# Kernel tuning notes

Hardware: AMD Instinct MI355X
Metric: run time of the kernel (lower is better)

## Reference

```python
import jax, jax.numpy as jnp
import numpy as np

E, D, H, W = 512, 64, 64, 64
B, L = 8, 2048
STEPS = 5
OUT_SIGMA_SCALE = 2.0


def setup_inputs() -> dict:
    key = jax.random.key(0)
    ks = jax.random.split(key, 8)
    tokens = jax.random.normal(ks[0], (B, L, E), dtype=jnp.float32)
    # positions on the HxW lattice: col 0 in [0,H), col 1 in [0,W)
    pos = jax.random.uniform(ks[1], (B, L, 2), dtype=jnp.float32)
    positions = pos * jnp.array([H, W], dtype=jnp.float32)
    # learned params (fan-in scaled init, as nn.Linear/Conv2d would give)
    W_to_field = jax.random.normal(ks[2], (D, E), dtype=jnp.float32) / np.sqrt(E)
    W_from_field = jax.random.normal(ks[3], (E, D), dtype=jnp.float32) / np.sqrt(D)
    conv1_w = jax.random.normal(ks[4], (2 * D, D, 3, 3), dtype=jnp.float32) / np.sqrt(D * 9)
    conv1_b = jnp.zeros((2 * D,), dtype=jnp.float32)
    conv2_w = jax.random.normal(ks[5], (D, 2 * D, 1, 1), dtype=jnp.float32) / np.sqrt(2 * D)
    conv2_b = jnp.zeros((D,), dtype=jnp.float32)
    log_sigma = jnp.array(np.log(4.0), dtype=jnp.float32)
    return {
        "tokens": tokens, "positions": positions,
        "W_to_field": W_to_field, "W_from_field": W_from_field,
        "conv1_w": conv1_w, "conv1_b": conv1_b,
        "conv2_w": conv2_w, "conv2_b": conv2_b,
        "log_sigma": log_sigma,
    }


def _conv2d(x, w, b, pad):
    y = jax.lax.conv_general_dilated(
        x, w, window_strides=(1, 1), padding=[(pad, pad), (pad, pad)],
        dimension_numbers=("NCHW", "OIHW", "NCHW"))
    return y + b[None, :, None, None]


def _norm_gauss(dy2, dx2, sigma):
    # (B,L,H,1)+(B,L,1,W) -> (B,L,H,W), normalized over the lattice
    g = jnp.exp(-(dy2 + dx2) / (2.0 * sigma * sigma))
    return g / (jnp.sum(g, axis=(-2, -1), keepdims=True) + 1e-6)


def reference(tokens, positions, W_to_field, W_from_field,
              conv1_w, conv1_b, conv2_w, conv2_b, log_sigma):
    sigma_in = jax.nn.softplus(log_sigma) + 1e-6
    sigma_out = sigma_in * OUT_SIGMA_SCALE

    proj = jnp.einsum("ble,de->bld", tokens, W_to_field)  # (B,L,D)

    grid_y = jnp.arange(H, dtype=jnp.float32)  # (H,)
    grid_x = jnp.arange(W, dtype=jnp.float32)  # (W,)
    dy2 = (grid_y[None, None, :, None] - positions[..., 0][..., None, None]) ** 2  # (B,L,H,1)
    dx2 = (grid_x[None, None, None, :] - positions[..., 1][..., None, None]) ** 2  # (B,L,1,W)

    weights_in = _norm_gauss(dy2, dx2, sigma_in)   # (B,L,H,W)
    field = jnp.einsum("blc,blhw->bchw", proj, weights_in)  # (B,D,H,W)

    for _ in range(STEPS):
        h = jax.nn.relu(_conv2d(field, conv1_w, conv1_b, pad=1))
        field = field + _conv2d(h, conv2_w, conv2_b, pad=0)

    weights_out = _norm_gauss(dy2, dx2, sigma_out)  # (B,L,H,W)
    sampled = jnp.einsum("bchw,blhw->blc", field, weights_out)  # (B,L,D)

    tokens_out = jnp.einsum("bld,ed->ble", sampled, W_from_field)  # (B,L,E)
    return tokens_out
```

## Files before the change

kernel.cpp:

```cpp
#include <hip/hip_runtime.h>
#include <cmath>
#include <cstddef>

#define BB 8
#define LL 2048
#define EE 512
#define HW 4096

typedef __attribute__((ext_vector_type(8))) short short8;
typedef __attribute__((ext_vector_type(4))) short short4v;
typedef __attribute__((ext_vector_type(4))) float f32x4;

__device__ __forceinline__ int swz(int row, int k, int ldk) {
    int g = (k >> 3) ^ (row & ((ldk >> 3) - 1));
    return row * ldk + (g << 3) + (k & 7);
}
__device__ __forceinline__ unsigned short f2bf(float f) {
    unsigned u = __builtin_bit_cast(unsigned, f);
    return (unsigned short)((u + 0x7FFFu + ((u >> 16) & 1u)) >> 16);
}
__device__ __forceinline__ float bf2f(short s) {
    return __builtin_bit_cast(float, (unsigned)((unsigned short)s) << 16);
}
__device__ __forceinline__ short4v cvt4(float4 v) {
    short4v r;
    r[0] = (short)f2bf(v.x); r[1] = (short)f2bf(v.y);
    r[2] = (short)f2bf(v.z); r[3] = (short)f2bf(v.w);
    return r;
}
#define MFMA16(acc, a, b) acc = __builtin_amdgcn_mfma_f32_16x16x32_bf16(a, b, acc, 0, 0, 0)

__global__ __launch_bounds__(256) void k_gauss(const float* __restrict__ pos,
        const float* __restrict__ lsig,
        short* __restrict__ gyiT, short* __restrict__ gxiT,
        short* __restrict__ gyoT, short* __restrict__ gxo,
        const float* __restrict__ w1, const float* __restrict__ w2,
        short* __restrict__ w1b, short* __restrict__ w2b) {
    __shared__ float red[4][4][64];
    __shared__ float tile[64 * 65];
    int t = threadIdx.x;
    int bx = blockIdx.x;
    {
        int i = bx * 256 + t;
        if (i < 73728) {
            int c = i & 63, o = (i >> 6) & 127, tap = i >> 13;
            w1b[i] = (short)f2bf(w1[(size_t)o * 576 + c * 9 + tap]);
        }
        if (i < 8192) w2b[i] = (short)f2bf(w2[i]);
    }
    if (bx >= 256) return;
    int ll = t & 63, q = t >> 6;
    int b = bx >> 5, lt = bx & 31;
    int bl = b * LL + lt * 64 + ll;
    float py = pos[(size_t)bl * 2 + 0];
    float px = pos[(size_t)bl * 2 + 1];
    float ls = lsig[0];
    float si = log1pf(expf(ls)) + 1e-6f;
    float so = si * 2.0f;
    float ai = 0.5f / (si * si), ao = 0.5f / (so * so);
    float vyi[16], vxi[16], vyo[16], vxo[16];
    float pyi = 0.f, pxi = 0.f, pyo = 0.f, pxo = 0.f;
    #pragma unroll
    for (int j = 0; j < 16; j++) {
        float g = (float)(q * 16 + j);
        float dy = g - py, dx = g - px;
        float dy2 = dy * dy, dx2 = dx * dx;
        vyi[j] = expf(-dy2 * ai); pyi += vyi[j];
        vxi[j] = expf(-dx2 * ai); pxi += vxi[j];
        vyo[j] = expf(-dy2 * ao); pyo += vyo[j];
        vxo[j] = expf(-dx2 * ao); pxo += vxo[j];
    }
    red[0][q][ll] = pyi; red[1][q][ll] = pxi;
    red[2][q][ll] = pyo; red[3][q][ll] = pxo;
    __syncthreads();
    float syi = red[0][0][ll] + red[0][1][ll] + red[0][2][ll] + red[0][3][ll];
    float sxi = red[1][0][ll] + red[1][1][ll] + red[1][2][ll] + red[1][3][ll];
    float syo = red[2][0][ll] + red[2][1][ll] + red[2][2][ll] + red[2][3][ll];
    float sxo = red[3][0][ll] + red[3][1][ll] + red[3][2][ll] + red[3][3][ll];
    float inv_i = 1.0f / (syi * sxi + 1e-6f);
    float inv_o = 1.0f / (syo * sxo + 1e-6f);
    size_t base = (size_t)b * 64 * LL + lt * 64 + ll;
    #pragma unroll
    for (int j = 0; j < 16; j++) {
        size_t off = base + (size_t)(q * 16 + j) * LL;
        gyiT[off] = (short)f2bf(vyi[j] * inv_i);
        gxiT[off] = (short)f2bf(vxi[j]);
        gyoT[off] = (short)f2bf(vyo[j] * inv_o);
        tile[(q * 16 + j) * 65 + ll] = vxo[j];
    }
    __syncthreads();
    #pragma unroll
    for (int j = 0; j < 16; j++) {
        int i = t + 256 * j;
        int lo = i >> 6, wo = i & 63;
        gxo[((size_t)b * LL + lt * 64 + lo) * 64 + wo] = (short)f2bf(tile[wo * 65 + lo]);
    }
}

__global__ __launch_bounds__(256) void k_proj(const float* __restrict__ tokens,
        const float* __restrict__ wtf, short* __restrict__ projT) {
    __shared__ __align__(16) short At[4096], Bt[4096];
    int t = threadIdx.x, lane = t & 63, wid = t >> 6;
    int blk = blockIdx.x;
    int b = blk >> 5;
    int l0b = (blk & 31) * 64;
    size_t tokbase = ((size_t)b * LL + l0b) * EE;
    f32x4 z = {0.f, 0.f, 0.f, 0.f};
    f32x4 acc[4] = {z, z, z, z};
    float4 pa[4], pb[4];
    #pragma unroll
    for (int j = 0; j < 4; j++) {
        int idx = t + 256 * j;
        int row = idx >> 4, kq = (idx & 15) << 2;
        pa[j] = *(const float4*)&wtf[(size_t)row * EE + kq];
        pb[j] = *(const float4*)&tokens[tokbase + (size_t)row * EE + kq];
    }
    for (int c = 0; c < 8; c++) {
        __syncthreads();
        #pragma unroll
        for (int j = 0; j < 4; j++) {
            int idx = t + 256 * j;
            int row = idx >> 4, kq = (idx & 15) << 2;
            *(short4v*)&At[swz(row, kq, 64)] = cvt4(pa[j]);
            *(short4v*)&Bt[swz(row, kq, 64)] = cvt4(pb[j]);
        }
        __syncthreads();
        if (c < 7) {
            int e0 = (c + 1) * 64;
            #pragma unroll
            for (int j = 0; j < 4; j++) {
                int idx = t + 256 * j;
                int row = idx >> 4, kq = (idx & 15) << 2;
                pa[j] = *(const float4*)&wtf[(size_t)row * EE + e0 + kq];
                pb[j] = *(const float4*)&tokens[tokbase + (size_t)row * EE + e0 + kq];
            }
        }
        int mrow = wid * 16 + (lane & 15);
        #pragma unroll
        for (int ks = 0; ks < 2; ks++) {
            int k0 = ks * 32 + (lane >> 4) * 8;
            short8 a = *(short8*)&At[swz(mrow, k0, 64)];
            #pragma unroll
            for (int n = 0; n < 4; n++) {
                short8 bb = *(short8*)&Bt[swz(n * 16 + (lane & 15), k0, 64)];
                MFMA16(acc[n], a, bb);
            }
        }
    }
    #pragma unroll
    for (int n = 0; n < 4; n++)
        #pragma unroll
        for (int r = 0; r < 4; r++) {
            int d = wid * 16 + ((lane >> 4) << 2) + r;
            int l = l0b + n * 16 + (lane & 15);
            projT[((size_t)b * 64 + d) * LL + l] = (short)f2bf(acc[n][r]);
        }
}

__global__ __launch_bounds__(256, 3) void k_scatter(const short* __restrict__ projT,
        const short* __restrict__ gyiT, const short* __restrict__ gxiT,
        float* __restrict__ fz) {
    __shared__ __align__(16) char smem[49152];
    short* At = (short*)smem;
    short* B0 = At + 8192;
    short* B1 = B0 + 8192;
    float* Cf = (float*)smem;
    const size_t FP = (size_t)BB * 64 * HW;
    int t = threadIdx.x, lane = t & 63, wid = t >> 6;
    int hp = blockIdx.x, b = blockIdx.y, kz = blockIdx.z;
    int h0 = hp * 2;
    const short* pj  = projT + (size_t)b * 64 * LL + kz * 1024;
    const short* gx  = gxiT + (size_t)b * 64 * LL + kz * 1024;
    const short* gy0 = gyiT + ((size_t)b * 64 + h0) * LL + kz * 1024;
    const short* gy1 = gy0 + LL;
    f32x4 z = {0.f, 0.f, 0.f, 0.f};
    f32x4 acc0[4] = {z, z, z, z}, acc1[4] = {z, z, z, z};
    int row_ = t >> 4, g_ = t & 15;
    short8 pA[4], pX[4], pY0v, pY1v;
    pY0v = *(const short8*)&gy0[g_ * 8];
    pY1v = *(const short8*)&gy1[g_ * 8];
    #pragma unroll
    for (int j = 0; j < 4; j++) {
        int row = row_ + 16 * j;
        pA[j] = *(const short8*)&pj[(size_t)row * LL + g_ * 8];
        pX[j] = *(const short8*)&gx[(size_t)row * LL + g_ * 8];
    }
    for (int c = 0; c < 8; c++) {
        __syncthreads();
        #pragma unroll
        for (int j = 0; j < 4; j++) {
            int row = row_ + 16 * j;
            short8 b0v, b1v;
            #pragma unroll
            for (int e = 0; e < 8; e++) {
                float gxv = bf2f(pX[j][e]);
                b0v[e] = (short)f2bf(gxv * bf2f(pY0v[e]));
                b1v[e] = (short)f2bf(gxv * bf2f(pY1v[e]));
            }
            *(short8*)&At[swz(row, g_ * 8, 128)] = pA[j];
            *(short8*)&B0[swz(row, g_ * 8, 128)] = b0v;
            *(short8*)&B1[swz(row, g_ * 8, 128)] = b1v;
        }
        __syncthreads();
        if (c < 7) {
            int off = (c + 1) * 128;
            pY0v = *(const short8*)&gy0[off + g_ * 8];
            pY1v = *(const short8*)&gy1[off + g_ * 8];
            #pragma unroll
            for (int j = 0; j < 4; j++) {
                int row = row_ + 16 * j;
                pA[j] = *(const short8*)&pj[(size_t)row * LL + off + g_ * 8];
                pX[j] = *(const short8*)&gx[(size_t)row * LL + off + g_ * 8];
            }
        }
        int mrow = wid * 16 + (lane & 15);
        #pragma unroll
        for (int ks = 0; ks < 4; ks++) {
            int k0 = ks * 32 + (lane >> 4) * 8;
            short8 a = *(short8*)&At[swz(mrow, k0, 128)];
            #pragma unroll
            for (int n = 0; n < 4; n++) {
                short8 b0f = *(short8*)&B0[swz(n * 16 + (lane & 15), k0, 128)];
                short8 b1f = *(short8*)&B1[swz(n * 16 + (lane & 15), k0, 128)];
                MFMA16(acc0[n], a, b0f);
                MFMA16(acc1[n], a, b1f);
            }
        }
    }
    float* dst = fz + (size_t)kz * FP;
    #pragma unroll
    for (int p = 0; p < 2; p++) {
        __syncthreads();
        #pragma unroll
        for (int n = 0; n < 4; n++)
            #pragma unroll
            for (int r = 0; r < 4; r++) {
                int w = n * 16 + (lane & 15);
                int cc = wid * 16 + ((lane >> 4) << 2) + r;
                Cf[w * 68 + cc] = (p == 0) ? acc0[n][r] : acc1[n][r];
            }
        __syncthreads();
        #pragma unroll
        for (int j = 0; j < 4; j++) {
            int i = t + 256 * j;
            int wo = i >> 4, cq = (i & 15) << 2;
            *(float4*)&dst[(((size_t)b * 64 + h0 + p) * 64 + wo) * 64 + cq] =
                *(float4*)&Cf[wo * 68 + cq];
        }
    }
}

__global__ __launch_bounds__(256, 3) void k_conv(const float* __restrict__ fin,
        int nparts, float* __restrict__ fout,
        const short* __restrict__ w1b, const float* __restrict__ b1,
        const short* __restrict__ w2b, const float* __restrict__ b2,
        short* __restrict__ fnchw, int final_step) {
    __shared__ __align__(16) char smem[45568];
    short* halo = (short*)smem;
    short* w1t  = (short*)(smem + 12800);
    short* ht   = (short*)(smem + 29184);
    float* Cf   = (float*)smem;
    const size_t FP = (size_t)BB * 64 * HW;
    int t = threadIdx.x, lane = t & 63, wid = t >> 6;
    int tile = blockIdx.x, b = blockIdx.y;
    int y0 = (tile >> 3) << 3, x0 = (tile & 7) << 3;
    const float* fb = fin + (size_t)b * 64 * HW;

    short8 w2f[4][4];
    #pragma unroll
    for (int n = 0; n < 4; n++)
        #pragma unroll
        for (int ks = 0; ks < 4; ks++)
            w2f[n][ks] = *(const short8*)&w2b[(size_t)(n * 16 + (lane & 15)) * 128
                                              + ks * 32 + (lane >> 4) * 8];
    short8 pf[4];
    #pragma unroll
    for (int j = 0; j < 4; j++) {
        int i = t + 256 * j; int o = i >> 3, g = i & 7;
        pf[j] = *(const short8*)&w1b[(size_t)o * 64 + g * 8];
    }
    for (int i = t; i < 1600; i += 256) {
        int pix = i >> 4, cq = (i & 15) << 2;
        int pr = pix / 10, pc = pix - pr * 10;
        int gy = y0 + pr - 1, gx = x0 + pc - 1;
        float4 v = {0.f, 0.f, 0.f, 0.f};
        if ((unsigned)gy < 64u && (unsigned)gx < 64u) {
            size_t a = ((size_t)gy * 64 + gx) * 64 + cq;
            v = *(const float4*)&fb[a];
            for (int p = 1; p < nparts; p++) {
                float4 u = *(const float4*)&fb[(size_t)p * FP + a];
                v.x += u.x; v.y += u.y; v.z += u.z; v.w += u.w;
            }
        }
        *(short4v*)&halo[swz(pix, cq, 64)] = cvt4(v);
    }
    f32x4 accH[8];
    #pragma unroll
    for (int n = 0; n < 8; n++) {
        float bv = b1[n * 16 + (lane & 15)];
        f32x4 v = {bv, bv, bv, bv};
        accH[n] = v;
    }
    int mpix = wid * 16 + (lane & 15);
    int ppy = mpix >> 3, ppx = mpix & 7;

    #pragma unroll
    for (int tap = 0; tap < 9; tap++) {
        #pragma unroll
        for (int j = 0; j < 4; j++) {
            int i = t + 256 * j; int o = i >> 3, g = i & 7;
            *(short8*)&w1t[swz(o, g * 8, 64)] = pf[j];
        }
        if (tap < 8) {
            #pragma unroll
            for (int j = 0; j < 4; j++) {
                int i = t + 256 * j; int o = i >> 3, g = i & 7;
                pf[j] = *(const short8*)&w1b[((size_t)(tap + 1) * 128 + o) * 64 + g * 8];
            }
        }
        __syncthreads();
        int ky = tap / 3, kx = tap - ky * 3;
        int hpix = (ppy + ky) * 10 + (ppx + kx);
        #pragma unroll
        for (int ks = 0; ks < 2; ks++) {
            int k0 = ks * 32 + (lane >> 4) * 8;
            short8 a = *(short8*)&halo[swz(hpix, k0, 64)];
            #pragma unroll
            for (int n = 0; n < 8; n++) {
                short8 bb = *(short8*)&w1t[swz(n * 16 + (lane & 15), k0, 64)];
                MFMA16(accH[n], a, bb);
            }
        }
        __syncthreads();
    }
    #pragma unroll
    for (int n = 0; n < 8; n++)
        #pragma unroll
        for (int r = 0; r < 4; r++) {
            int m = wid * 16 + ((lane >> 4) << 2) + r;
            int o = n * 16 + (lane & 15);
            ht[swz(m, o, 128)] = (short)f2bf(fmaxf(accH[n][r], 0.f));
        }
    __syncthreads();
    f32x4 acc2[4];
    #pragma unroll
    for (int n = 0; n < 4; n++) {
        float bv = b2[n * 16 + (lane & 15)];
        f32x4 v = {bv, bv, bv, bv};
        acc2[n] = v;
    }
    #pragma unroll
    for (int ks = 0; ks < 4; ks++) {
        int k0 = ks * 32 + (lane >> 4) * 8;
        short8 a = *(short8*)&ht[swz(mpix, k0, 128)];
        #pragma unroll
        for (int n = 0; n < 4; n++) MFMA16(acc2[n], a, w2f[n][ks]);
    }
    float* fo = fout + (size_t)b * 64 * HW;
    #pragma unroll
    for (int n = 0; n < 4; n++)
        #pragma unroll
        for (int r = 0; r < 4; r++) {
            int m = wid * 16 + ((lane >> 4) << 2) + r;
            int py = m >> 3, px = m & 7;
            int d = n * 16 + (lane & 15);
            size_t a = (((size_t)(y0 + py)) * 64 + x0 + px) * 64 + d;
            float fv = fb[a];
            for (int p = 1; p < nparts; p++) fv += fb[(size_t)p * FP + a];
            float val = acc2[n][r] + fv;
            if (!final_step) fo[a] = val;
            else Cf[d * 68 + m] = val;
        }
    if (final_step) {
        __syncthreads();
        #pragma unroll
        for (int j = 0; j < 4; j++) {
            int i = t + 256 * j;
            int d = i >> 4, pq = (i & 15) << 2;
            int py = pq >> 3, px = pq & 7;
            float4 v = *(float4*)&Cf[d * 68 + pq];
            *(short4v*)&fnchw[(((size_t)b * 64 + d) * 64 + y0 + py) * 64 + x0 + px] =
                cvt4(v);
        }
    }
}

__global__ __launch_bounds__(256, 4) void k_gather(const short* __restrict__ fnchw,
        const short* __restrict__ gyoT, const short* __restrict__ gxo,
        float* __restrict__ sampz) {
    __shared__ __align__(16) short At[8192], Bt[8192];
    int t = threadIdx.x, lane = t & 63, wid = t >> 6;
    int lt = blockIdx.x, b = blockIdx.y, zz = blockIdx.z;
    int l0 = lt * 64;
    f32x4 z4 = {0.f, 0.f, 0.f, 0.f};
    f32x4 acc[4] = {z4, z4, z4, z4};
    int row_ = t >> 4, g_ = t & 15;
    int hl_ = g_ >> 3, w8_ = (g_ & 7) * 8;
    short8 pX[4], pB[4];
    float pY[4];
    #pragma unroll
    for (int j = 0; j < 4; j++) {
        int row = row_ + 16 * j;
        int h = zz * 16 + hl_;
        pX[j] = *(const short8*)&gxo[((size_t)b * LL + l0 + row) * 64 + w8_];
        pY[j] = bf2f(gyoT[((size_t)b * 64 + h) * LL + l0 + row]);
        pB[j] = *(const short8*)&fnchw[(((size_t)b * 64 + row) * 64 + h) * 64 + w8_];
    }
    for (int c = 0; c < 8; c++) {
        __syncthreads();
        #pragma unroll
        for (int j = 0; j < 4; j++) {
            int row = row_ + 16 * j;
            short8 a;
            #pragma unroll
            for (int e = 0; e < 8; e++)
                a[e] = (short)f2bf(bf2f(pX[j][e]) * pY[j]);
            *(short8*)&At[swz(row, g_ * 8, 128)] = a;
            *(short8*)&Bt[swz(row, g_ * 8, 128)] = pB[j];
        }
        __syncthreads();
        if (c < 7) {
            int h = zz * 16 + (c + 1) * 2 + hl_;
            #pragma unroll
            for (int j = 0; j < 4; j++) {
                int row = row_ + 16 * j;
                pY[j] = bf2f(gyoT[((size_t)b * 64 + h) * LL + l0 + row]);
                pB[j] = *(const short8*)&fnchw[(((size_t)b * 64 + row) * 64 + h) * 64 + w8_];
            }
        }
        int mrow = wid * 16 + (lane & 15);
        #pragma unroll
        for (int ks = 0; ks < 4; ks++) {
            int k0 = ks * 32 + (lane >> 4) * 8;
            short8 a = *(short8*)&At[swz(mrow, k0, 128)];
            #pragma unroll
            for (int n = 0; n < 4; n++) {
                short8 bb = *(short8*)&Bt[swz(n * 16 + (lane & 15), k0, 128)];
                MFMA16(acc[n], a, bb);
            }
        }
    }
    #pragma unroll
    for (int n = 0; n < 4; n++)
        #pragma unroll
        for (int r = 0; r < 4; r++) {
            int lr = wid * 16 + ((lane >> 4) << 2) + r;
            int cc = n * 16 + (lane & 15);
            sampz[(((size_t)zz * BB + b) * LL + l0 + lr) * 64 + cc] = acc[n][r];
        }
}

__global__ __launch_bounds__(256) void k_out(const float* __restrict__ samp,
        const float* __restrict__ wff, float* __restrict__ out) {
    __shared__ __align__(16) short At[4096], Bt[4096];
    const size_t SP = 1048576;
    int t = threadIdx.x, lane = t & 63, wid = t >> 6;
    int mt = blockIdx.x, e0 = blockIdx.y * 64;
    #pragma unroll
    for (int j = 0; j < 4; j++) {
        int idx = t + 256 * j;
        int row = idx >> 4, kq = (idx & 15) << 2;
        size_t off = ((size_t)mt * 64 + row) * 64 + kq;
        float4 v0 = *(const float4*)&samp[off];
        float4 v1 = *(const float4*)&samp[off + SP];
        float4 v2 = *(const float4*)&samp[off + 2 * SP];
        float4 v3 = *(const float4*)&samp[off + 3 * SP];
        float4 vs = {v0.x + v1.x + v2.x + v3.x, v0.y + v1.y + v2.y + v3.y,
                     v0.z + v1.z + v2.z + v3.z, v0.w + v1.w + v2.w + v3.w};
        *(short4v*)&At[swz(row, kq, 64)] = cvt4(vs);
        float4 wv = *(const float4*)&wff[(size_t)(e0 + row) * 64 + kq];
        *(short4v*)&Bt[swz(row, kq, 64)] = cvt4(wv);
    }
    __syncthreads();
    f32x4 z = {0.f, 0.f, 0.f, 0.f};
    f32x4 acc[4] = {z, z, z, z};
    int mrow = wid * 16 + (lane & 15);
    #pragma unroll
    for (int ks = 0; ks < 2; ks++) {
        int k0 = ks * 32 + (lane >> 4) * 8;
        short8 a = *(short8*)&At[swz(mrow, k0, 64)];
        #pragma unroll
        for (int n = 0; n < 4; n++) {
            short8 bb = *(short8*)&Bt[swz(n * 16 + (lane & 15), k0, 64)];
            MFMA16(acc[n], a, bb);
        }
    }
    #pragma unroll
    for (int n = 0; n < 4; n++)
        #pragma unroll
        for (int r = 0; r < 4; r++) {
            int lr = wid * 16 + ((lane >> 4) << 2) + r;
            int ec = e0 + n * 16 + (lane & 15);
            out[((size_t)mt * 64 + lr) * EE + ec] = acc[n][r];
        }
}

extern "C" void kernel_launch(void* const* d_in, const int* in_sizes, int n_in,
                              void* d_out, int out_size, void* d_ws, size_t ws_size,
                              hipStream_t stream) {
    const float* tokens = (const float*)d_in[0];
    const float* pos    = (const float*)d_in[1];
    const float* wtf    = (const float*)d_in[2];
    const float* wff    = (const float*)d_in[3];
    const float* w1     = (const float*)d_in[4];
    const float* b1     = (const float*)d_in[5];
    const float* w2     = (const float*)d_in[6];
    const float* b2     = (const float*)d_in[7];
    const float* lsig   = (const float*)d_in[8];
    float* out = (float*)d_out;

    const size_t M1 = 1048576;
    float* ws    = (float*)d_ws;
    short* sbase = (short*)d_ws;
    short* gyiT  = sbase;
    short* gxiT  = sbase + 1 * M1;
    short* gyoT  = sbase + 2 * M1;
    short* gxo   = sbase + 3 * M1;
    short* projT = sbase + 4 * M1;
    float* fz    = ws + 3 * M1;
    float* fA    = ws + 7 * M1;
    float* fB    = ws + 9 * M1;
    short* fnchw = (short*)(ws + 11 * M1);
    float* samp  = ws + 12 * M1;
    short* w1b   = (short*)(ws + 16 * M1);
    short* w2b   = w1b + 73728;

    hipLaunchKernelGGL(k_gauss, dim3(288), dim3(256), 0, stream,
                       pos, lsig, gyiT, gxiT, gyoT, gxo, w1, w2, w1b, w2b);
    hipLaunchKernelGGL(k_proj, dim3(256), dim3(256), 0, stream, tokens, wtf, projT);
    hipLaunchKernelGGL(k_scatter, dim3(32, 8, 2), dim3(256), 0, stream,
                       projT, gyiT, gxiT, fz);
    hipLaunchKernelGGL(k_conv, dim3(64, 8), dim3(256), 0, stream,
                       fz, 2, fB, w1b, b1, w2b, b2, fnchw, 0);
    hipLaunchKernelGGL(k_conv, dim3(64, 8), dim3(256), 0, stream,
                       fB, 1, fA, w1b, b1, w2b, b2, fnchw, 0);
    hipLaunchKernelGGL(k_conv, dim3(64, 8), dim3(256), 0, stream,
                       fA, 1, fB, w1b, b1, w2b, b2, fnchw, 0);
    hipLaunchKernelGGL(k_conv, dim3(64, 8), dim3(256), 0, stream,
                       fB, 1, fA, w1b, b1, w2b, b2, fnchw, 0);
    hipLaunchKernelGGL(k_conv, dim3(64, 8), dim3(256), 0, stream,
                       fA, 1, fB, w1b, b1, w2b, b2, fnchw, 1);
    hipLaunchKernelGGL(k_gather, dim3(32, 8, 4), dim3(256), 0, stream,
                       fnchw, gyoT, gxo, samp);
    hipLaunchKernelGGL(k_out, dim3(256, 8), dim3(256), 0, stream,
                       samp, wff, out);
}
```

Baseline: 244.1 us.

## Fuse projection into gauss kernel and double split-K for scatter and gather

Merges the token projection GEMM into the gaussian-weights kernel as extra blocks, so both run in one launch and can overlap. Doubles the split-K factor of the scatter kernel (2 to 4 partial fields) and of the gather kernel (4 to 8 partial samples) to launch more blocks on a large GPU. In exchange, the conv and output kernels must read and sum more partial buffers, and the fused kernel's larger shared memory footprint may lower occupancy of the gauss blocks.

```diff
diff --git a/kernel.cpp b/kernel.cpp
--- a/kernel.cpp
+++ b/kernel.cpp
@@ -30,16 +30,79 @@
 }
 #define MFMA16(acc, a, b) acc = __builtin_amdgcn_mfma_f32_16x16x32_bf16(a, b, acc, 0, 0, 0)
 
-__global__ __launch_bounds__(256) void k_gauss(const float* __restrict__ pos,
+__global__ __launch_bounds__(256) void k_gauss_proj(const float* __restrict__ pos,
         const float* __restrict__ lsig,
         short* __restrict__ gyiT, short* __restrict__ gxiT,
         short* __restrict__ gyoT, short* __restrict__ gxo,
         const float* __restrict__ w1, const float* __restrict__ w2,
-        short* __restrict__ w1b, short* __restrict__ w2b) {
+        short* __restrict__ w1b, short* __restrict__ w2b,
+        const float* __restrict__ tokens, const float* __restrict__ wtf,
+        short* __restrict__ projT) {
     __shared__ float red[4][4][64];
     __shared__ float tile[64 * 65];
+    __shared__ __align__(16) short At[4096], Bt[4096];
     int t = threadIdx.x;
     int bx = blockIdx.x;
+
+    if (bx >= 288) {
+        int blk = bx - 288;
+        int lane = t & 63, wid = t >> 6;
+        int b = blk >> 5;
+        int l0b = (blk & 31) * 64;
+        size_t tokbase = ((size_t)b * LL + l0b) * EE;
+        f32x4 z = {0.f, 0.f, 0.f, 0.f};
+        f32x4 acc[4] = {z, z, z, z};
+        float4 pa[4], pb[4];
+        #pragma unroll
+        for (int j = 0; j < 4; j++) {
+            int idx = t + 256 * j;
+            int row = idx >> 4, kq = (idx & 15) << 2;
+            pa[j] = *(const float4*)&wtf[(size_t)row * EE + kq];
+            pb[j] = *(const float4*)&tokens[tokbase + (size_t)row * EE + kq];
+        }
+        for (int c = 0; c < 8; c++) {
+            __syncthreads();
+            #pragma unroll
+            for (int j = 0; j < 4; j++) {
+                int idx = t + 256 * j;
+                int row = idx >> 4, kq = (idx & 15) << 2;
+                *(short4v*)&At[swz(row, kq, 64)] = cvt4(pa[j]);
+                *(short4v*)&Bt[swz(row, kq, 64)] = cvt4(pb[j]);
+            }
+            __syncthreads();
+            if (c < 7) {
+                int e0 = (c + 1) * 64;
+                #pragma unroll
+                for (int j = 0; j < 4; j++) {
+                    int idx = t + 256 * j;
+                    int row = idx >> 4, kq = (idx & 15) << 2;
+                    pa[j] = *(const float4*)&wtf[(size_t)row * EE + e0 + kq];
+                    pb[j] = *(const float4*)&tokens[tokbase + (size_t)row * EE + e0 + kq];
+                }
+            }
+            int mrow = wid * 16 + (lane & 15);
+            #pragma unroll
+            for (int ks = 0; ks < 2; ks++) {
+                int k0 = ks * 32 + (lane >> 4) * 8;
+                short8 a = *(short8*)&At[swz(mrow, k0, 64)];
+                #pragma unroll
+                for (int n = 0; n < 4; n++) {
+                    short8 bb = *(short8*)&Bt[swz(n * 16 + (lane & 15), k0, 64)];
+                    MFMA16(acc[n], a, bb);
+                }
+            }
+        }
+        #pragma unroll
+        for (int n = 0; n < 4; n++)
+            #pragma unroll
+            for (int r = 0; r < 4; r++) {
+                int d = wid * 16 + ((lane >> 4) << 2) + r;
+                int l = l0b + n * 16 + (lane & 15);
+                projT[((size_t)b * 64 + d) * LL + l] = (short)f2bf(acc[n][r]);
+            }
+        return;
+    }
+
     {
         int i = bx * 256 + t;
         if (i < 73728) {
@@ -97,66 +160,6 @@
     }
 }
 
-__global__ __launch_bounds__(256) void k_proj(const float* __restrict__ tokens,
-        const float* __restrict__ wtf, short* __restrict__ projT) {
-    __shared__ __align__(16) short At[4096], Bt[4096];
-    int t = threadIdx.x, lane = t & 63, wid = t >> 6;
-    int blk = blockIdx.x;
-    int b = blk >> 5;
-    int l0b = (blk & 31) * 64;
-    size_t tokbase = ((size_t)b * LL + l0b) * EE;
-    f32x4 z = {0.f, 0.f, 0.f, 0.f};
-    f32x4 acc[4] = {z, z, z, z};
-    float4 pa[4], pb[4];
-    #pragma unroll
-    for (int j = 0; j < 4; j++) {
-        int idx = t + 256 * j;
-        int row = idx >> 4, kq = (idx & 15) << 2;
-        pa[j] = *(const float4*)&wtf[(size_t)row * EE + kq];
-        pb[j] = *(const float4*)&tokens[tokbase + (size_t)row * EE + kq];
-    }
-    for (int c = 0; c < 8; c++) {
-        __syncthreads();
-        #pragma unroll
-        for (int j = 0; j < 4; j++) {
-            int idx = t + 256 * j;
-            int row = idx >> 4, kq = (idx & 15) << 2;
-            *(short4v*)&At[swz(row, kq, 64)] = cvt4(pa[j]);
-            *(short4v*)&Bt[swz(row, kq, 64)] = cvt4(pb[j]);
-        }
-        __syncthreads();
-        if (c < 7) {
-            int e0 = (c + 1) * 64;
-            #pragma unroll
-            for (int j = 0; j < 4; j++) {
-                int idx = t + 256 * j;
-                int row = idx >> 4, kq = (idx & 15) << 2;
-                pa[j] = *(const float4*)&wtf[(size_t)row * EE + e0 + kq];
-                pb[j] = *(const float4*)&tokens[tokbase + (size_t)row * EE + e0 + kq];
-            }
-        }
-        int mrow = wid * 16 + (lane & 15);
-        #pragma unroll
-        for (int ks = 0; ks < 2; ks++) {
-            int k0 = ks * 32 + (lane >> 4) * 8;
-            short8 a = *(short8*)&At[swz(mrow, k0, 64)];
-            #pragma unroll
-            for (int n = 0; n < 4; n++) {
-                short8 bb = *(short8*)&Bt[swz(n * 16 + (lane & 15), k0, 64)];
-                MFMA16(acc[n], a, bb);
-            }
-        }
-    }
-    #pragma unroll
-    for (int n = 0; n < 4; n++)
-        #pragma unroll
-        for (int r = 0; r < 4; r++) {
-            int d = wid * 16 + ((lane >> 4) << 2) + r;
-            int l = l0b + n * 16 + (lane & 15);
-            projT[((size_t)b * 64 + d) * LL + l] = (short)f2bf(acc[n][r]);
-        }
-}
-
 __global__ __launch_bounds__(256, 3) void k_scatter(const short* __restrict__ projT,
         const short* __restrict__ gyiT, const short* __restrict__ gxiT,
         float* __restrict__ fz) {
@@ -169,9 +172,9 @@
     int t = threadIdx.x, lane = t & 63, wid = t >> 6;
     int hp = blockIdx.x, b = blockIdx.y, kz = blockIdx.z;
     int h0 = hp * 2;
-    const short* pj  = projT + (size_t)b * 64 * LL + kz * 1024;
-    const short* gx  = gxiT + (size_t)b * 64 * LL + kz * 1024;
-    const short* gy0 = gyiT + ((size_t)b * 64 + h0) * LL + kz * 1024;
+    const short* pj  = projT + (size_t)b * 64 * LL + kz * 512;
+    const short* gx  = gxiT + (size_t)b * 64 * LL + kz * 512;
+    const short* gy0 = gyiT + ((size_t)b * 64 + h0) * LL + kz * 512;
     const short* gy1 = gy0 + LL;
     f32x4 z = {0.f, 0.f, 0.f, 0.f};
     f32x4 acc0[4] = {z, z, z, z}, acc1[4] = {z, z, z, z};
@@ -185,7 +188,7 @@
         pA[j] = *(const short8*)&pj[(size_t)row * LL + g_ * 8];
         pX[j] = *(const short8*)&gx[(size_t)row * LL + g_ * 8];
     }
-    for (int c = 0; c < 8; c++) {
+    for (int c = 0; c < 4; c++) {
         __syncthreads();
         #pragma unroll
         for (int j = 0; j < 4; j++) {
@@ -202,7 +205,7 @@
             *(short8*)&B1[swz(row, g_ * 8, 128)] = b1v;
         }
         __syncthreads();
-        if (c < 7) {
+        if (c < 3) {
             int off = (c + 1) * 128;
             pY0v = *(const short8*)&gy0[off + g_ * 8];
             pY1v = *(const short8*)&gy1[off + g_ * 8];
@@ -401,12 +404,12 @@
     #pragma unroll
     for (int j = 0; j < 4; j++) {
         int row = row_ + 16 * j;
-        int h = zz * 16 + hl_;
+        int h = zz * 8 + hl_;
         pX[j] = *(const short8*)&gxo[((size_t)b * LL + l0 + row) * 64 + w8_];
         pY[j] = bf2f(gyoT[((size_t)b * 64 + h) * LL + l0 + row]);
         pB[j] = *(const short8*)&fnchw[(((size_t)b * 64 + row) * 64 + h) * 64 + w8_];
     }
-    for (int c = 0; c < 8; c++) {
+    for (int c = 0; c < 4; c++) {
         __syncthreads();
         #pragma unroll
         for (int j = 0; j < 4; j++) {
@@ -419,8 +422,8 @@
             *(short8*)&Bt[swz(row, g_ * 8, 128)] = pB[j];
         }
         __syncthreads();
-        if (c < 7) {
-            int h = zz * 16 + (c + 1) * 2 + hl_;
+        if (c < 3) {
+            int h = zz * 8 + (c + 1) * 2 + hl_;
             #pragma unroll
             for (int j = 0; j < 4; j++) {
                 int row = row_ + 16 * j;
@@ -461,12 +464,12 @@
         int idx = t + 256 * j;
         int row = idx >> 4, kq = (idx & 15) << 2;
         size_t off = ((size_t)mt * 64 + row) * 64 + kq;
-        float4 v0 = *(const float4*)&samp[off];
-        float4 v1 = *(const float4*)&samp[off + SP];
-        float4 v2 = *(const float4*)&samp[off + 2 * SP];
-        float4 v3 = *(const float4*)&samp[off + 3 * SP];
-        float4 vs = {v0.x + v1.x + v2.x + v3.x, v0.y + v1.y + v2.y + v3.y,
-                     v0.z + v1.z + v2.z + v3.z, v0.w + v1.w + v2.w + v3.w};
+        float4 vs = {0.f, 0.f, 0.f, 0.f};
+        #pragma unroll
+        for (int zp = 0; zp < 8; zp++) {
+            float4 v = *(const float4*)&samp[off + (size_t)zp * SP];
+            vs.x += v.x; vs.y += v.y; vs.z += v.z; vs.w += v.w;
+        }
         *(short4v*)&At[swz(row, kq, 64)] = cvt4(vs);
         float4 wv = *(const float4*)&wff[(size_t)(e0 + row) * 64 + kq];
         *(short4v*)&Bt[swz(row, kq, 64)] = cvt4(wv);
@@ -518,20 +521,20 @@
     short* gxo   = sbase + 3 * M1;
     short* projT = sbase + 4 * M1;
     float* fz    = ws + 3 * M1;
-    float* fA    = ws + 7 * M1;
-    float* fB    = ws + 9 * M1;
-    short* fnchw = (short*)(ws + 11 * M1);
-    float* samp  = ws + 12 * M1;
-    short* w1b   = (short*)(ws + 16 * M1);
+    float* fA    = ws + 11 * M1;
+    float* fB    = ws + 13 * M1;
+    short* fnchw = (short*)(ws + 15 * M1);
+    float* samp  = ws + 16 * M1;
+    short* w1b   = (short*)(ws + 24 * M1);
     short* w2b   = w1b + 73728;
 
-    hipLaunchKernelGGL(k_gauss, dim3(288), dim3(256), 0, stream,
-                       pos, lsig, gyiT, gxiT, gyoT, gxo, w1, w2, w1b, w2b);
-    hipLaunchKernelGGL(k_proj, dim3(256), dim3(256), 0, stream, tokens, wtf, projT);
-    hipLaunchKernelGGL(k_scatter, dim3(32, 8, 2), dim3(256), 0, stream,
+    hipLaunchKernelGGL(k_gauss_proj, dim3(544), dim3(256), 0, stream,
+                       pos, lsig, gyiT, gxiT, gyoT, gxo, w1, w2, w1b, w2b,
+                       tokens, wtf, projT);
+    hipLaunchKernelGGL(k_scatter, dim3(32, 8, 4), dim3(256), 0, stream,
                        projT, gyiT, gxiT, fz);
     hipLaunchKernelGGL(k_conv, dim3(64, 8), dim3(256), 0, stream,
-                       fz, 2, fB, w1b, b1, w2b, b2, fnchw, 0);
+                       fz, 4, fB, w1b, b1, w2b, b2, fnchw, 0);
     hipLaunchKernelGGL(k_conv, dim3(64, 8), dim3(256), 0, stream,
                        fB, 1, fA, w1b, b1, w2b, b2, fnchw, 0);
     hipLaunchKernelGGL(k_conv, dim3(64, 8), dim3(256), 0, stream,
@@ -540,7 +543,7 @@
                        fB, 1, fA, w1b, b1, w2b, b2, fnchw, 0);
     hipLaunchKernelGGL(k_conv, dim3(64, 8), dim3(256), 0, stream,
                        fA, 1, fB, w1b, b1, w2b, b2, fnchw, 1);
-    hipLaunchKernelGGL(k_gather, dim3(32, 8, 4), dim3(256), 0, stream,
+    hipLaunchKernelGGL(k_gather, dim3(32, 8, 8), dim3(256), 0, stream,
                        fnchw, gyoT, gxo, samp);
     hipLaunchKernelGGL(k_out, dim3(256, 8), dim3(256), 0, stream,
                        samp, wff, out);
```

Result: slower. 268.0 us (+9.8%).

## Merge gauss and projection kernels; put batch index fastest in grid order

Applied to the files above, without the earlier changes.

The projection GEMM now runs inside the Gaussian-table kernel as extra blocks (index 288 and up), so the two independent stages share one launch and can overlap. Every other kernel now takes the batch index from blockIdx.x, which reorders block dispatch so consecutive blocks span different batches. The merged kernel's shared memory grows to hold both stages' buffers, which may lower occupancy, and the new dispatch order changes L2 and XCD locality in ways that are hard to predict.

```diff
diff --git a/kernel.cpp b/kernel.cpp
--- a/kernel.cpp
+++ b/kernel.cpp
@@ -30,16 +30,79 @@
 }
 #define MFMA16(acc, a, b) acc = __builtin_amdgcn_mfma_f32_16x16x32_bf16(a, b, acc, 0, 0, 0)
 
-__global__ __launch_bounds__(256) void k_gauss(const float* __restrict__ pos,
+__global__ __launch_bounds__(256) void k_gauss_proj(const float* __restrict__ pos,
         const float* __restrict__ lsig,
         short* __restrict__ gyiT, short* __restrict__ gxiT,
         short* __restrict__ gyoT, short* __restrict__ gxo,
         const float* __restrict__ w1, const float* __restrict__ w2,
-        short* __restrict__ w1b, short* __restrict__ w2b) {
+        short* __restrict__ w1b, short* __restrict__ w2b,
+        const float* __restrict__ tokens, const float* __restrict__ wtf,
+        short* __restrict__ projT) {
     __shared__ float red[4][4][64];
     __shared__ float tile[64 * 65];
+    __shared__ __align__(16) short At[4096], Bt[4096];
     int t = threadIdx.x;
     int bx = blockIdx.x;
+
+    if (bx >= 288) {
+        int blk = bx - 288;
+        int lane = t & 63, wid = t >> 6;
+        int b = blk >> 5;
+        int l0b = (blk & 31) * 64;
+        size_t tokbase = ((size_t)b * LL + l0b) * EE;
+        f32x4 z = {0.f, 0.f, 0.f, 0.f};
+        f32x4 acc[4] = {z, z, z, z};
+        float4 pa[4], pb[4];
+        #pragma unroll
+        for (int j = 0; j < 4; j++) {
+            int idx = t + 256 * j;
+            int row = idx >> 4, kq = (idx & 15) << 2;
+            pa[j] = *(const float4*)&wtf[(size_t)row * EE + kq];
+            pb[j] = *(const float4*)&tokens[tokbase + (size_t)row * EE + kq];
+        }
+        for (int c = 0; c < 8; c++) {
+            __syncthreads();
+            #pragma unroll
+            for (int j = 0; j < 4; j++) {
+                int idx = t + 256 * j;
+                int row = idx >> 4, kq = (idx & 15) << 2;
+                *(short4v*)&At[swz(row, kq, 64)] = cvt4(pa[j]);
+                *(short4v*)&Bt[swz(row, kq, 64)] = cvt4(pb[j]);
+            }
+            __syncthreads();
+            if (c < 7) {
+                int e0 = (c + 1) * 64;
+                #pragma unroll
+                for (int j = 0; j < 4; j++) {
+                    int idx = t + 256 * j;
+                    int row = idx >> 4, kq = (idx & 15) << 2;
+                    pa[j] = *(const float4*)&wtf[(size_t)row * EE + e0 + kq];
+                    pb[j] = *(const float4*)&tokens[tokbase + (size_t)row * EE + e0 + kq];
+                }
+            }
+            int mrow = wid * 16 + (lane & 15);
+            #pragma unroll
+            for (int ks = 0; ks < 2; ks++) {
+                int k0 = ks * 32 + (lane >> 4) * 8;
+                short8 a = *(short8*)&At[swz(mrow, k0, 64)];
+                #pragma unroll
+                for (int n = 0; n < 4; n++) {
+                    short8 bb = *(short8*)&Bt[swz(n * 16 + (lane & 15), k0, 64)];
+                    MFMA16(acc[n], a, bb);
+                }
+            }
+        }
+        #pragma unroll
+        for (int n = 0; n < 4; n++)
+            #pragma unroll
+            for (int r = 0; r < 4; r++) {
+                int d = wid * 16 + ((lane >> 4) << 2) + r;
+                int l = l0b + n * 16 + (lane & 15);
+                projT[((size_t)b * 64 + d) * LL + l] = (short)f2bf(acc[n][r]);
+            }
+        return;
+    }
+
     {
         int i = bx * 256 + t;
         if (i < 73728) {
@@ -97,66 +160,6 @@
     }
 }
 
-__global__ __launch_bounds__(256) void k_proj(const float* __restrict__ tokens,
-        const float* __restrict__ wtf, short* __restrict__ projT) {
-    __shared__ __align__(16) short At[4096], Bt[4096];
-    int t = threadIdx.x, lane = t & 63, wid = t >> 6;
-    int blk = blockIdx.x;
-    int b = blk >> 5;
-    int l0b = (blk & 31) * 64;
-    size_t tokbase = ((size_t)b * LL + l0b) * EE;
-    f32x4 z = {0.f, 0.f, 0.f, 0.f};
-    f32x4 acc[4] = {z, z, z, z};
-    float4 pa[4], pb[4];
-    #pragma unroll
-    for (int j = 0; j < 4; j++) {
-        int idx = t + 256 * j;
-        int row = idx >> 4, kq = (idx & 15) << 2;
-        pa[j] = *(const float4*)&wtf[(size_t)row * EE + kq];
-        pb[j] = *(const float4*)&tokens[tokbase + (size_t)row * EE + kq];
-    }
-    for (int c = 0; c < 8; c++) {
-        __syncthreads();
-        #pragma unroll
-        for (int j = 0; j < 4; j++) {
-            int idx = t + 256 * j;
-            int row = idx >> 4, kq = (idx & 15) << 2;
-            *(short4v*)&At[swz(row, kq, 64)] = cvt4(pa[j]);
-            *(short4v*)&Bt[swz(row, kq, 64)] = cvt4(pb[j]);
-        }
-        __syncthreads();
-        if (c < 7) {
-            int e0 = (c + 1) * 64;
-            #pragma unroll
-            for (int j = 0; j < 4; j++) {
-                int idx = t + 256 * j;
-                int row = idx >> 4, kq = (idx & 15) << 2;
-                pa[j] = *(const float4*)&wtf[(size_t)row * EE + e0 + kq];
-                pb[j] = *(const float4*)&tokens[tokbase + (size_t)row * EE + e0 + kq];
-            }
-        }
-        int mrow = wid * 16 + (lane & 15);
-        #pragma unroll
-        for (int ks = 0; ks < 2; ks++) {
-            int k0 = ks * 32 + (lane >> 4) * 8;
-            short8 a = *(short8*)&At[swz(mrow, k0, 64)];
-            #pragma unroll
-            for (int n = 0; n < 4; n++) {
-                short8 bb = *(short8*)&Bt[swz(n * 16 + (lane & 15), k0, 64)];
-                MFMA16(acc[n], a, bb);
-            }
-        }
-    }
-    #pragma unroll
-    for (int n = 0; n < 4; n++)
-        #pragma unroll
-        for (int r = 0; r < 4; r++) {
-            int d = wid * 16 + ((lane >> 4) << 2) + r;
-            int l = l0b + n * 16 + (lane & 15);
-            projT[((size_t)b * 64 + d) * LL + l] = (short)f2bf(acc[n][r]);
-        }
-}
-
 __global__ __launch_bounds__(256, 3) void k_scatter(const short* __restrict__ projT,
         const short* __restrict__ gyiT, const short* __restrict__ gxiT,
         float* __restrict__ fz) {
@@ -167,7 +170,7 @@
     float* Cf = (float*)smem;
     const size_t FP = (size_t)BB * 64 * HW;
     int t = threadIdx.x, lane = t & 63, wid = t >> 6;
-    int hp = blockIdx.x, b = blockIdx.y, kz = blockIdx.z;
+    int b = blockIdx.x, hp = blockIdx.y, kz = blockIdx.z;
     int h0 = hp * 2;
     const short* pj  = projT + (size_t)b * 64 * LL + kz * 1024;
     const short* gx  = gxiT + (size_t)b * 64 * LL + kz * 1024;
@@ -262,7 +265,7 @@
     float* Cf   = (float*)smem;
     const size_t FP = (size_t)BB * 64 * HW;
     int t = threadIdx.x, lane = t & 63, wid = t >> 6;
-    int tile = blockIdx.x, b = blockIdx.y;
+    int b = blockIdx.x, tile = blockIdx.y;
     int y0 = (tile >> 3) << 3, x0 = (tile & 7) << 3;
     const float* fb = fin + (size_t)b * 64 * HW;
 
@@ -390,7 +393,7 @@
         float* __restrict__ sampz) {
     __shared__ __align__(16) short At[8192], Bt[8192];
     int t = threadIdx.x, lane = t & 63, wid = t >> 6;
-    int lt = blockIdx.x, b = blockIdx.y, zz = blockIdx.z;
+    int b = blockIdx.x, lt = blockIdx.y, zz = blockIdx.z;
     int l0 = lt * 64;
     f32x4 z4 = {0.f, 0.f, 0.f, 0.f};
     f32x4 acc[4] = {z4, z4, z4, z4};
@@ -455,7 +458,8 @@
     __shared__ __align__(16) short At[4096], Bt[4096];
     const size_t SP = 1048576;
     int t = threadIdx.x, lane = t & 63, wid = t >> 6;
-    int mt = blockIdx.x, e0 = blockIdx.y * 64;
+    int b = blockIdx.x, mtl = blockIdx.y, ez = blockIdx.z;
+    int mt = b * 32 + mtl, e0 = ez * 64;
     #pragma unroll
     for (int j = 0; j < 4; j++) {
         int idx = t + 256 * j;
@@ -525,23 +529,23 @@
     short* w1b   = (short*)(ws + 16 * M1);
     short* w2b   = w1b + 73728;
 
-    hipLaunchKernelGGL(k_gauss, dim3(288), dim3(256), 0, stream,
-                       pos, lsig, gyiT, gxiT, gyoT, gxo, w1, w2, w1b, w2b);
-    hipLaunchKernelGGL(k_proj, dim3(256), dim3(256), 0, stream, tokens, wtf, projT);
-    hipLaunchKernelGGL(k_scatter, dim3(32, 8, 2), dim3(256), 0, stream,
+    hipLaunchKernelGGL(k_gauss_proj, dim3(544), dim3(256), 0, stream,
+                       pos, lsig, gyiT, gxiT, gyoT, gxo, w1, w2, w1b, w2b,
+                       tokens, wtf, projT);
+    hipLaunchKernelGGL(k_scatter, dim3(8, 32, 2), dim3(256), 0, stream,
                        projT, gyiT, gxiT, fz);
-    hipLaunchKernelGGL(k_conv, dim3(64, 8), dim3(256), 0, stream,
+    hipLaunchKernelGGL(k_conv, dim3(8, 64), dim3(256), 0, stream,
                        fz, 2, fB, w1b, b1, w2b, b2, fnchw, 0);
-    hipLaunchKernelGGL(k_conv, dim3(64, 8), dim3(256), 0, stream,
+    hipLaunchKernelGGL(k_conv, dim3(8, 64), dim3(256), 0, stream,
                        fB, 1, fA, w1b, b1, w2b, b2, fnchw, 0);
-    hipLaunchKernelGGL(k_conv, dim3(64, 8), dim3(256), 0, stream,
+    hipLaunchKernelGGL(k_conv, dim3(8, 64), dim3(256), 0, stream,
                        fA, 1, fB, w1b, b1, w2b, b2, fnchw, 0);
-    hipLaunchKernelGGL(k_conv, dim3(64, 8), dim3(256), 0, stream,
+    hipLaunchKernelGGL(k_conv, dim3(8, 64), dim3(256), 0, stream,
                        fB, 1, fA, w1b, b1, w2b, b2, fnchw, 0);
-    hipLaunchKernelGGL(k_conv, dim3(64, 8), dim3(256), 0, stream,
+    hipLaunchKernelGGL(k_conv, dim3(8, 64), dim3(256), 0, stream,
                        fA, 1, fB, w1b, b1, w2b, b2, fnchw, 1);
-    hipLaunchKernelGGL(k_gather, dim3(32, 8, 4), dim3(256), 0, stream,
+    hipLaunchKernelGGL(k_gather, dim3(8, 32, 4), dim3(256), 0, stream,
                        fnchw, gyoT, gxo, samp);
-    hipLaunchKernelGGL(k_out, dim3(256, 8), dim3(256), 0, stream,
+    hipLaunchKernelGGL(k_out, dim3(8, 32, 8), dim3(256), 0, stream,
                        samp, wff, out);
 }
```

Result: faster. 237.9 us (-2.6%).
